# Optimization experiments

Measured on AMD Instinct MI355X. Metric: run time of the kernel, lower is better.

The kernel has to match this reference:

```python
import jax, jax.numpy as jnp
import numpy as np
from jax import lax


def _leaky(x):
    # LeakyReLU, negative_slope=0.1
    return jnp.where(x > 0, x, 0.1 * x)


def _conv(x, w, pad, groups=1):
    # NCHW / OIHW 2D conv, stride 1
    return lax.conv_general_dilated(
        x, w, (1, 1), [(pad, pad), (pad, pad)],
        dimension_numbers=("NCHW", "OIHW", "NCHW"),
        feature_group_count=groups)


def setup_inputs() -> dict:
    key = jax.random.key(0)
    ks = jax.random.split(key, 12)
    B, C, H, W = 16, 64, 256, 256
    KS = 3

    def nrm(k, shape, fan_in):
        return jax.random.normal(k, shape, jnp.float32) / np.float32(np.sqrt(fan_in))

    return {
        "x": jax.random.normal(ks[0], (B, C, H, W), jnp.float32),
        "t": jax.random.normal(ks[1], (B, 1, 1, 1), jnp.float32),
        # t_process: 1x1 convs (1->64, 64->64), no bias -> stored as matrices
        "tW1": nrm(ks[2], (C, 1), 1),
        "tW2": nrm(ks[3], (C, C), C),
        # f_process: two 3x3 convs 64->64 with bias
        "fW1": nrm(ks[4], (C, C, KS, KS), C * KS * KS),
        "fb1": jnp.zeros((C,), jnp.float32),
        "fW2": nrm(ks[5], (C, C, KS, KS), C * KS * KS),
        "fb2": jnp.zeros((C,), jnp.float32),
        # kernel branch: 1x1 convs (1->64, 64->64*9), no bias
        "kW1": nrm(ks[6], (C, 1), 1),
        "kW2": nrm(ks[7], (C * KS * KS, C), C),
        # conv33: 3x3 conv 64->64 with bias
        "cW": nrm(ks[8], (C, C, KS, KS), C * KS * KS),
        "cb": jnp.zeros((C,), jnp.float32),
    }


def reference(x, t, tW1, tW2, fW1, fb1, fW2, fb2, kW1, kW2, cW, cb):
    b, c, h, w = x.shape
    KS = 3

    # f_process: Conv3x3 -> LeakyReLU -> Conv3x3 -> LeakyReLU
    f = _leaky(_conv(x, fW1, 1) + fb1[None, :, None, None])
    f = _leaky(_conv(f, fW2, 1) + fb2[None, :, None, None])

    # t is (b,1,1,1); 1x1 convs on it are per-sample matmuls
    ts = t.reshape(b, 1)
    # t_process: Conv1x1 -> LeakyReLU -> Conv1x1 -> Sigmoid -> (b,c,1,1)
    mv = jax.nn.sigmoid(_leaky(ts @ tW1.T) @ tW2.T).reshape(b, c, 1, 1)

    # kernel branch: Conv1x1 -> LeakyReLU -> Conv1x1 -> LeakyReLU -> (b*c,1,3,3)
    kern = _leaky(_leaky(ts @ kW1.T) @ kW2.T).reshape(b * c, 1, KS, KS)

    # per-sample-channel dynamic depthwise conv: groups = b*c
    out = _conv(f.reshape(1, b * c, h, w), kern, (KS - 1) // 2,
                groups=b * c).reshape(b, c, h, w)

    # modulation gating + residual 3x3 conv
    return out * mv + _conv(x, cW, 1) + cb[None, :, None, None]
```

## Files before the change

kernel.cpp:

```cpp
#include <hip/hip_runtime.h>
#include <cstdint>

using short8  = __attribute__((ext_vector_type(8))) short;
using short4v = __attribute__((ext_vector_type(4))) short;
using f32x16  = __attribute__((ext_vector_type(16))) float;
using float4v = __attribute__((ext_vector_type(4))) float;
typedef unsigned short ushort_t;

#define CHUNK_ROW 520
#define CHUNK_SLOTS 1560
#define BUF_SLOTS 1632
#define BUF_SHORTS (BUF_SLOTS * 8)

__device__ __forceinline__ float lrelu(float x) { return x > 0.f ? x : 0.1f * x; }

__device__ __forceinline__ ushort_t f2bf(float f) {
    union { float f; unsigned u; } v; v.f = f;
    unsigned r = (v.u + 0x7FFFu + ((v.u >> 16) & 1u)) >> 16;
    return (ushort_t)r;
}
__device__ __forceinline__ float bf2f(ushort_t b) {
    union { unsigned u; float f; } v; v.u = ((unsigned)b) << 16; return v.f;
}

__device__ __forceinline__ void gload_lds16(const ushort_t* g, ushort_t* l) {
    __builtin_amdgcn_global_load_lds(
        (const __attribute__((address_space(1))) void*)g,
        (__attribute__((address_space(3))) void*)l, 16, 0, 0);
}

__global__ void k_tiny(const float* __restrict__ t, const float* __restrict__ tW1,
                       const float* __restrict__ tW2, const float* __restrict__ kW1,
                       const float* __restrict__ kW2, float* __restrict__ ktr) {
    int b = blockIdx.x;
    int c = threadIdx.x;
    __shared__ float h1[64], g1[64];
    float ts = t[b];
    h1[c] = lrelu(ts * tW1[c]);
    g1[c] = lrelu(ts * kW1[c]);
    __syncthreads();
    float s = 0.f;
    for (int j = 0; j < 64; ++j) s = fmaf(tW2[c * 64 + j], h1[j], s);
    float mvv = 1.f / (1.f + expf(-s));
    for (int q = 0; q < 9; ++q) {
        float s2 = 0.f;
        for (int j = 0; j < 64; ++j) s2 = fmaf(kW2[(c * 9 + q) * 64 + j], g1[j], s2);
        ktr[b * 576 + q * 64 + c] = lrelu(s2) * mvv;
    }
}

__global__ void k_zrow(ushort_t* __restrict__ z) {
    int i = blockIdx.x * 256 + threadIdx.x;
    *(short8*)(z + (size_t)i * 8) = (short8)0;
}

__global__ void k_pack(const float* __restrict__ w1, const float* __restrict__ w2,
                       const float* __restrict__ w3, ushort_t* __restrict__ wp) {
    int idx = blockIdx.x * 256 + threadIdx.x;
    if (idx >= 3 * 36864) return;
    int conv = idx / 36864, r = idx % 36864;
    const float* W = conv == 0 ? w1 : (conv == 1 ? w2 : w3);
    int j = r & 7, lane = (r >> 3) & 63, ct = (r >> 9) & 1, chunk = (r >> 10) & 3,
        t = r >> 12;
    int co = ct * 32 + (lane & 31);
    int ci = chunk * 16 + (lane >> 5) * 8 + j;
    wp[idx] = f2bf(W[(co * 64 + ci) * 9 + t]);
}

__global__ __launch_bounds__(256) void k_tr(const float* __restrict__ x,
                                            ushort_t* __restrict__ xbf) {
    int bid = blockIdx.x;
    int h = bid & 255, b = bid >> 8;
    int t = threadIdx.x;
    for (int it = 0; it < 8; ++it) {
        int idx = t + it * 256;
        int g = idx & 7, w = idx >> 3;
        const float* src = x + (((size_t)(b * 64 + g * 8) * 256 + h) * 256 + w);
        short8 v;
#pragma unroll
        for (int j = 0; j < 8; ++j) v[j] = (short)f2bf(src[(size_t)j * 65536]);
        *(short8*)(xbf + (((size_t)(b * 256 + h) * 256 + w) * 64 + g * 8)) = v;
    }
}

#define STAGE_CHUNK(chunk, bufbase)                                              \
    {                                                                            \
        _Pragma("unroll")                                                        \
        for (int i_ = 0; i_ < 7; ++i_) {                                         \
            int base_ = wv * 390 + i_ * 64;                                      \
            int S_ = base_ + lane;                                               \
            S_ = S_ < CHUNK_SLOTS ? S_ : CHUNK_SLOTS - 1;                        \
            int row_ = (S_ >= 2 * CHUNK_ROW) ? 2 : (S_ >= CHUNK_ROW ? 1 : 0);    \
            int rem_ = S_ - row_ * CHUNK_ROW;                                    \
            int mg_ = rem_ >> 3, sl_ = rem_ & 7;                                 \
            int sp_ = sl_ ^ (mg_ & 7);                                           \
            int p_ = mg_ * 4 + (sp_ >> 1), g_ = sp_ & 1;                         \
            int wsx_ = p_ - 1;                                                   \
            bool edge_ = (unsigned)wsx_ >= 256u;                                 \
            const ushort_t* rp_ = (row_ == 0) ? rb0 : (row_ == 1 ? rb1 : rb2);   \
            const ushort_t* src_ =                                               \
                edge_ ? zv : (rp_ + wsx_ * 64 + (chunk)*16 + g_ * 8);            \
            gload_lds16(src_, xs + (bufbase) + (size_t)base_ * 8);               \
        }                                                                        \
    }

#define VMCNT(n) asm volatile("s_waitcnt vmcnt(" #n ")" ::: "memory")
#define RBAR() __builtin_amdgcn_s_barrier()

__global__ __launch_bounds__(256, 2) void k_conv13(
    const ushort_t* __restrict__ in, const ushort_t* __restrict__ zv,
    const ushort_t* __restrict__ wpa, const ushort_t* __restrict__ wpc,
    const float* __restrict__ ba, const float* __restrict__ bc,
    ushort_t* __restrict__ f1out, float* __restrict__ cres) {
    __shared__ __align__(16) ushort_t xs[2 * BUF_SHORTS];
    const int tid = threadIdx.x;
    const int lane = tid & 63;
    const int wv = tid >> 6;
    const unsigned bid = blockIdx.x;
    const unsigned L = (bid & 7u) * 512u + (bid >> 3);
    const int h = L & 255, b = L >> 8;
    const int l31 = lane & 31, lhi = lane >> 5;
    const int pw0 = wv * 64;

    const ushort_t* rb0 = (h > 0)   ? in + ((size_t)(b * 256 + h - 1)) * 16384 : zv;
    const ushort_t* rb1 =             in + ((size_t)(b * 256 + h)) * 16384;
    const ushort_t* rb2 = (h < 255) ? in + ((size_t)(b * 256 + h + 1)) * 16384 : zv;

    f32x16 accA[2][2], accC[2][2];
#pragma unroll
    for (int a = 0; a < 2; ++a)
#pragma unroll
        for (int c = 0; c < 2; ++c) { accA[a][c] = (f32x16)0.0f; accC[a][c] = (f32x16)0.0f; }

#define COMPUTE13(chunk, bufbase)                                                   \
    {                                                                               \
        __builtin_amdgcn_s_setprio(1);                                              \
        _Pragma("unroll")                                                           \
        for (int t_ = 0; t_ < 9; ++t_) {                                            \
            const int dwx_ = t_ % 3, rr_ = t_ / 3;                                  \
            const int off_ = ((t_ * 4 + (chunk)) * 2) * 512 + lane * 8;             \
            short8 a0 = *(const short8*)(wpa + off_);                               \
            short8 a1 = *(const short8*)(wpa + off_ + 512);                         \
            short8 c0 = *(const short8*)(wpc + off_);                               \
            short8 c1 = *(const short8*)(wpc + off_ + 512);                         \
            _Pragma("unroll")                                                       \
            for (int pt_ = 0; pt_ < 2; ++pt_) {                                     \
                int p_ = pw0 + pt_ * 32 + l31 + dwx_;                               \
                int mg_ = p_ >> 2;                                                  \
                int sl_ = ((p_ & 3) * 2 + lhi) ^ (mg_ & 7);                         \
                short8 bf = *(const short8*)(                                       \
                    xs + (bufbase) + (size_t)(rr_ * CHUNK_ROW + mg_ * 8 + sl_) * 8);\
                accA[0][pt_] = __builtin_amdgcn_mfma_f32_32x32x16_bf16(a0, bf, accA[0][pt_], 0, 0, 0); \
                accA[1][pt_] = __builtin_amdgcn_mfma_f32_32x32x16_bf16(a1, bf, accA[1][pt_], 0, 0, 0); \
                accC[0][pt_] = __builtin_amdgcn_mfma_f32_32x32x16_bf16(c0, bf, accC[0][pt_], 0, 0, 0); \
                accC[1][pt_] = __builtin_amdgcn_mfma_f32_32x32x16_bf16(c1, bf, accC[1][pt_], 0, 0, 0); \
            }                                                                       \
        }                                                                           \
        __builtin_amdgcn_s_setprio(0);                                              \
    }

    STAGE_CHUNK(0, 0);
    STAGE_CHUNK(1, BUF_SHORTS);
    VMCNT(7);
    RBAR();
    COMPUTE13(0, 0);
    RBAR();
    STAGE_CHUNK(2, 0);
    VMCNT(7);
    RBAR();
    COMPUTE13(1, BUF_SHORTS);
    RBAR();
    STAGE_CHUNK(3, BUF_SHORTS);
    VMCNT(7);
    RBAR();
    COMPUTE13(2, 0);
    RBAR();
    VMCNT(0);
    RBAR();
    COMPUTE13(3, BUF_SHORTS);

    const int co_b = 4 * lhi;
    {
        ushort_t* outb = f1out + ((size_t)(b * 256 + h)) * 16384;
#pragma unroll
        for (int ct = 0; ct < 2; ++ct)
#pragma unroll
            for (int pt = 0; pt < 2; ++pt) {
                int pix = pw0 + pt * 32 + l31;
                ushort_t* po = outb + (size_t)pix * 64 + ct * 32 + co_b;
#pragma unroll
                for (int q = 0; q < 4; ++q) {
                    float4v bv = *(const float4v*)(ba + ct * 32 + co_b + 8 * q);
                    short4v sv;
#pragma unroll
                    for (int m = 0; m < 4; ++m) {
                        float v = lrelu(accA[ct][pt][q * 4 + m] + bv[m]);
                        sv[m] = (short)f2bf(v);
                    }
                    *(short4v*)(po + 8 * q) = sv;
                }
            }
    }
    {
        float* pb = cres + (((size_t)b * 64) << 16) + h * 256;
#pragma unroll
        for (int ct = 0; ct < 2; ++ct)
#pragma unroll
            for (int pt = 0; pt < 2; ++pt) {
                int pix = pw0 + pt * 32 + l31;
#pragma unroll
                for (int q = 0; q < 4; ++q) {
                    float4v bv = *(const float4v*)(bc + ct * 32 + co_b + 8 * q);
#pragma unroll
                    for (int m = 0; m < 4; ++m) {
                        int c = ct * 32 + co_b + 8 * q + m;
                        pb[((size_t)c << 16) + pix] = accC[ct][pt][q * 4 + m] + bv[m];
                    }
                }
            }
    }
#undef COMPUTE13
}

__global__ __launch_bounds__(256, 3) void k_conv2(const ushort_t* __restrict__ in,
                                                  const ushort_t* __restrict__ zv,
                                                  const ushort_t* __restrict__ wp,
                                                  const float* __restrict__ bias,
                                                  ushort_t* __restrict__ outp) {
    __shared__ __align__(16) ushort_t xs[2 * BUF_SHORTS];
    const int tid = threadIdx.x;
    const int lane = tid & 63;
    const int wv = tid >> 6;
    const unsigned bid = blockIdx.x;
    const unsigned L = (bid & 7u) * 512u + (bid >> 3);
    const int h = L & 255, b = L >> 8;
    const int l31 = lane & 31, lhi = lane >> 5;
    const int pw0 = wv * 64;

    const ushort_t* rb0 = (h > 0)   ? in + ((size_t)(b * 256 + h - 1)) * 16384 : zv;
    const ushort_t* rb1 =             in + ((size_t)(b * 256 + h)) * 16384;
    const ushort_t* rb2 = (h < 255) ? in + ((size_t)(b * 256 + h + 1)) * 16384 : zv;

    f32x16 acc[2][2];
#pragma unroll
    for (int a = 0; a < 2; ++a)
#pragma unroll
        for (int c = 0; c < 2; ++c) acc[a][c] = (f32x16)0.0f;

#define COMPUTE2(chunk, bufbase)                                                    \
    {                                                                               \
        __builtin_amdgcn_s_setprio(1);                                              \
        _Pragma("unroll")                                                           \
        for (int t_ = 0; t_ < 9; ++t_) {                                            \
            const int dwx_ = t_ % 3, rr_ = t_ / 3;                                  \
            const int off_ = ((t_ * 4 + (chunk)) * 2) * 512 + lane * 8;             \
            short8 a0 = *(const short8*)(wp + off_);                                \
            short8 a1 = *(const short8*)(wp + off_ + 512);                          \
            _Pragma("unroll")                                                       \
            for (int pt_ = 0; pt_ < 2; ++pt_) {                                     \
                int p_ = pw0 + pt_ * 32 + l31 + dwx_;                               \
                int mg_ = p_ >> 2;                                                  \
                int sl_ = ((p_ & 3) * 2 + lhi) ^ (mg_ & 7);                         \
                short8 bf = *(const short8*)(                                       \
                    xs + (bufbase) + (size_t)(rr_ * CHUNK_ROW + mg_ * 8 + sl_) * 8);\
                acc[0][pt_] = __builtin_amdgcn_mfma_f32_32x32x16_bf16(a0, bf, acc[0][pt_], 0, 0, 0); \
                acc[1][pt_] = __builtin_amdgcn_mfma_f32_32x32x16_bf16(a1, bf, acc[1][pt_], 0, 0, 0); \
            }                                                                       \
        }                                                                           \
        __builtin_amdgcn_s_setprio(0);                                              \
    }

    STAGE_CHUNK(0, 0);
    STAGE_CHUNK(1, BUF_SHORTS);
    VMCNT(7);
    RBAR();
    COMPUTE2(0, 0);
    RBAR();
    STAGE_CHUNK(2, 0);
    VMCNT(7);
    RBAR();
    COMPUTE2(1, BUF_SHORTS);
    RBAR();
    STAGE_CHUNK(3, BUF_SHORTS);
    VMCNT(7);
    RBAR();
    COMPUTE2(2, 0);
    RBAR();
    VMCNT(0);
    RBAR();
    COMPUTE2(3, BUF_SHORTS);

    const int co_b = 4 * lhi;
    ushort_t* pb = outp + (((size_t)b * 64) << 16) + h * 256;
#pragma unroll
    for (int ct = 0; ct < 2; ++ct)
#pragma unroll
        for (int pt = 0; pt < 2; ++pt) {
            int pix = pw0 + pt * 32 + l31;
#pragma unroll
            for (int q = 0; q < 4; ++q) {
                float4v bv = *(const float4v*)(bias + ct * 32 + co_b + 8 * q);
#pragma unroll
                for (int m = 0; m < 4; ++m) {
                    int c = ct * 32 + co_b + 8 * q + m;
                    float v = lrelu(acc[ct][pt][q * 4 + m] + bv[m]);
                    pb[((size_t)c << 16) + pix] = f2bf(v);
                }
            }
        }
#undef COMPUTE2
}

__global__ __launch_bounds__(256) void k_fin(const ushort_t* __restrict__ f2,
                                             const float* __restrict__ ktr,
                                             float* __restrict__ out) {
    __shared__ __align__(16) ushort_t s[10 * 272];
    const unsigned bid = blockIdx.x;
    const unsigned L = (bid & 7u) * 4096u + (bid >> 3);
    const int hb = L & 31, c = (L >> 5) & 63, b = L >> 11;
    const int h0 = hb * 8;
    const int w = threadIdx.x;

    const ushort_t* f2c = f2 + (((size_t)(b * 64 + c)) << 16);
    for (int i = w; i < 320; i += 256) {
        int r = i >> 5, seg = i & 31;
        int hs = h0 - 1 + r;
        short8 v = (short8)0;
        if ((unsigned)hs < 256u) v = *(const short8*)(f2c + hs * 256 + seg * 8);
        *(short8*)(&s[r * 272 + 8 + seg * 8]) = v;
        if (seg == 0) s[r * 272 + 7] = 0;
        if (seg == 31) s[r * 272 + 264] = 0;
    }
    __syncthreads();

    float kv[9];
#pragma unroll
    for (int t9 = 0; t9 < 9; ++t9) kv[t9] = ktr[b * 576 + t9 * 64 + c];

    float lv[10], cv[10], rv[10];
#pragma unroll
    for (int r = 0; r < 10; ++r) {
        lv[r] = bf2f(s[r * 272 + 7 + w]);
        cv[r] = bf2f(s[r * 272 + 8 + w]);
        rv[r] = bf2f(s[r * 272 + 9 + w]);
    }

    float* ob = out + (((size_t)(b * 64 + c)) << 16) + h0 * 256 + w;
#pragma unroll
    for (int rr = 0; rr < 8; ++rr) {
        float dwv = 0.f;
#pragma unroll
        for (int r3 = 0; r3 < 3; ++r3) {
            dwv = fmaf(kv[r3 * 3 + 0], lv[rr + r3], dwv);
            dwv = fmaf(kv[r3 * 3 + 1], cv[rr + r3], dwv);
            dwv = fmaf(kv[r3 * 3 + 2], rv[rr + r3], dwv);
        }
        float* po = ob + rr * 256;
        *po = *po + dwv;
    }
}

extern "C" void kernel_launch(void* const* d_in, const int* in_sizes, int n_in,
                              void* d_out, int out_size, void* d_ws, size_t ws_size,
                              hipStream_t stream) {
    const float* x   = (const float*)d_in[0];
    const float* t   = (const float*)d_in[1];
    const float* tW1 = (const float*)d_in[2];
    const float* tW2 = (const float*)d_in[3];
    const float* fW1 = (const float*)d_in[4];
    const float* fb1 = (const float*)d_in[5];
    const float* fW2 = (const float*)d_in[6];
    const float* fb2 = (const float*)d_in[7];
    const float* kW1 = (const float*)d_in[8];
    const float* kW2 = (const float*)d_in[9];
    const float* cW  = (const float*)d_in[10];
    const float* cb  = (const float*)d_in[11];

    char* ws = (char*)d_ws;
    float*    ktr  = (float*)ws;
    ushort_t* wp   = (ushort_t*)(ws + 65536);
    ushort_t* zv   = (ushort_t*)(ws + 294912);
    ushort_t* xbf  = (ushort_t*)(ws + (512u << 10));
    ushort_t* f1bf = (ushort_t*)(ws + (512u << 10) + ((size_t)128 << 20));
    ushort_t* f2n  = xbf;
    float*    out  = (float*)d_out;

    k_tiny<<<dim3(16), dim3(64), 0, stream>>>(t, tW1, tW2, kW1, kW2, ktr);
    k_zrow<<<dim3(8), dim3(256), 0, stream>>>(zv);
    k_pack<<<dim3((3 * 36864 + 255) / 256), dim3(256), 0, stream>>>(fW1, fW2, cW, wp);
    k_tr<<<dim3(4096), dim3(256), 0, stream>>>(x, xbf);

    k_conv13<<<dim3(4096), dim3(256), 0, stream>>>(
        xbf, zv, wp, wp + 2 * 36864, fb1, cb, f1bf, out);
    k_conv2<<<dim3(4096), dim3(256), 0, stream>>>(f1bf, zv, wp + 36864, fb2, f2n);
    k_fin<<<dim3(32768), dim3(256), 0, stream>>>(f2n, ktr, out);
}
```

Baseline: 631.1 us.

## Compute two output rows per block and stage conv weights in LDS

Both 3x3 conv kernels now use 512-thread blocks that compute two adjacent output rows. They stage four input rows, so the shared rows are reused, and the block count is halved. Conv weights are repacked into chunk-major layout and loaded into LDS via global_load_lds (double-buffered per chunk for the fused conv1/conv3 kernel, fully resident for conv2) instead of being read from global memory by every wave. The aim is to cut redundant input-row and weight reads. The cost is much larger dynamic LDS, which may limit occupancy, and added barrier coordination.

```diff
diff --git a/kernel.cpp b/kernel.cpp
--- a/kernel.cpp
+++ b/kernel.cpp
@@ -7,10 +7,14 @@
 using float4v = __attribute__((ext_vector_type(4))) float;
 typedef unsigned short ushort_t;
 
-#define CHUNK_ROW 520
-#define CHUNK_SLOTS 1560
-#define BUF_SLOTS 1632
-#define BUF_SHORTS (BUF_SLOTS * 8)
+#define CSLOTS 2080
+#define BSLOTS 2144
+#define XSH (BSLOTS * 8)
+#define WROWS 40
+#define WCH (WROWS * 512)
+#define W1SH 36864
+#define DYN13 ((2 * WCH + 2 * XSH) * 2)
+#define DYN2  ((W1SH + 2 * XSH) * 2)
 
 __device__ __forceinline__ float lrelu(float x) { return x > 0.f ? x : 0.1f * x; }
 
@@ -28,6 +32,10 @@
         (const __attribute__((address_space(1))) void*)g,
         (__attribute__((address_space(3))) void*)l, 16, 0, 0);
 }
+
+#define VMCNT(n) asm volatile("s_waitcnt vmcnt(" #n ")" ::: "memory")
+#define RBAR() __builtin_amdgcn_s_barrier()
+#define SCHED0() __builtin_amdgcn_sched_barrier(0)
 
 __global__ void k_tiny(const float* __restrict__ t, const float* __restrict__ tW1,
                        const float* __restrict__ tW2, const float* __restrict__ kW1,
@@ -55,16 +63,37 @@
 }
 
 __global__ void k_pack(const float* __restrict__ w1, const float* __restrict__ w2,
-                       const float* __restrict__ w3, ushort_t* __restrict__ wp) {
+                       const float* __restrict__ w3, ushort_t* __restrict__ wpM,
+                       ushort_t* __restrict__ wp2) {
     int idx = blockIdx.x * 256 + threadIdx.x;
-    if (idx >= 3 * 36864) return;
-    int conv = idx / 36864, r = idx % 36864;
-    const float* W = conv == 0 ? w1 : (conv == 1 ? w2 : w3);
-    int j = r & 7, lane = (r >> 3) & 63, ct = (r >> 9) & 1, chunk = (r >> 10) & 3,
-        t = r >> 12;
+    const int NM = 4 * 36 * 512;
+    if (idx >= NM + 4 * 18 * 512) return;
+    const float* W;
+    ushort_t* dst;
+    int chunk, row;
+    int e;
+    if (idx < NM) {
+        chunk = idx / (36 * 512);
+        int rem = idx % (36 * 512);
+        row = rem / 512;
+        e = rem % 512;
+        W = (row < 18) ? w1 : w3;
+        dst = wpM + idx;
+        row %= 18;
+    } else {
+        int i2 = idx - NM;
+        chunk = i2 / (18 * 512);
+        int rem = i2 % (18 * 512);
+        row = rem / 512;
+        e = rem % 512;
+        W = w2;
+        dst = wp2 + i2;
+    }
+    int lane = e >> 3, j = e & 7;
+    int t = row >> 1, ct = row & 1;
     int co = ct * 32 + (lane & 31);
     int ci = chunk * 16 + (lane >> 5) * 8 + j;
-    wp[idx] = f2bf(W[(co * 64 + ci) * 9 + t]);
+    *dst = f2bf(W[(co * 64 + ci) * 9 + t]);
 }
 
 __global__ __launch_bounds__(256) void k_tr(const float* __restrict__ x,
@@ -83,48 +112,93 @@
     }
 }
 
-#define STAGE_CHUNK(chunk, bufbase)                                              \
+#define STAGE_X(chunk, xbase)                                                    \
     {                                                                            \
         _Pragma("unroll")                                                        \
-        for (int i_ = 0; i_ < 7; ++i_) {                                         \
-            int base_ = wv * 390 + i_ * 64;                                      \
+        for (int i_ = 0; i_ < 5; ++i_) {                                         \
+            int base_ = wv * 260 + i_ * 64;                                      \
             int S_ = base_ + lane;                                               \
-            S_ = S_ < CHUNK_SLOTS ? S_ : CHUNK_SLOTS - 1;                        \
-            int row_ = (S_ >= 2 * CHUNK_ROW) ? 2 : (S_ >= CHUNK_ROW ? 1 : 0);    \
-            int rem_ = S_ - row_ * CHUNK_ROW;                                    \
+            S_ = S_ < CSLOTS ? S_ : CSLOTS - 1;                                  \
+            int r_ = (S_ >= 1560) ? 3 : ((S_ >= 1040) ? 2 : ((S_ >= 520) ? 1 : 0)); \
+            int rem_ = S_ - r_ * 520;                                            \
             int mg_ = rem_ >> 3, sl_ = rem_ & 7;                                 \
             int sp_ = sl_ ^ (mg_ & 7);                                           \
             int p_ = mg_ * 4 + (sp_ >> 1), g_ = sp_ & 1;                         \
             int wsx_ = p_ - 1;                                                   \
             bool edge_ = (unsigned)wsx_ >= 256u;                                 \
-            const ushort_t* rp_ = (row_ == 0) ? rb0 : (row_ == 1 ? rb1 : rb2);   \
+            const ushort_t* rp_ =                                                \
+                (r_ == 0) ? rb0 : ((r_ == 1) ? rb1 : ((r_ == 2) ? rb2 : rb3));   \
             const ushort_t* src_ =                                               \
                 edge_ ? zv : (rp_ + wsx_ * 64 + (chunk)*16 + g_ * 8);            \
-            gload_lds16(src_, xs + (bufbase) + (size_t)base_ * 8);               \
+            gload_lds16(src_, xs + (xbase) + (size_t)base_ * 8);                 \
         }                                                                        \
     }
 
-#define VMCNT(n) asm volatile("s_waitcnt vmcnt(" #n ")" ::: "memory")
-#define RBAR() __builtin_amdgcn_s_barrier()
-
-__global__ __launch_bounds__(256, 2) void k_conv13(
+#define STAGE_W(chunk, wbase)                                                    \
+    {                                                                            \
+        _Pragma("unroll")                                                        \
+        for (int i_ = 0; i_ < 5; ++i_) {                                         \
+            int row_ = wv * 5 + i_;                                              \
+            int rc_ = row_ > 35 ? 35 : row_;                                     \
+            gload_lds16(wpM + (size_t)((chunk)*36 + rc_) * 512 + lane * 8,       \
+                        wlds + (wbase) + (size_t)row_ * 512);                    \
+        }                                                                        \
+    }
+
+__device__ __forceinline__ void computeM(const ushort_t* __restrict__ wlds,
+                                         const ushort_t* __restrict__ xs,
+                                         int wbase, int xbase, int lane, int pw0,
+                                         int l31, int lhi, int rbase,
+                                         f32x16 (&accA)[2][2], f32x16 (&accC)[2][2]) {
+    __builtin_amdgcn_s_setprio(1);
+#pragma unroll
+    for (int t = 0; t < 9; ++t) {
+        short8 a0 = *(const short8*)(wlds + wbase + (size_t)(t * 2 + 0) * 512 + lane * 8);
+        short8 a1 = *(const short8*)(wlds + wbase + (size_t)(t * 2 + 1) * 512 + lane * 8);
+        short8 c0 = *(const short8*)(wlds + wbase + (size_t)(18 + t * 2 + 0) * 512 + lane * 8);
+        short8 c1 = *(const short8*)(wlds + wbase + (size_t)(18 + t * 2 + 1) * 512 + lane * 8);
+        const int dwx = t % 3, rr = t / 3;
+        const int rowIdx = rbase + rr;
+#pragma unroll
+        for (int pt = 0; pt < 2; ++pt) {
+            int p = pw0 + pt * 32 + l31 + dwx;
+            int mg = p >> 2;
+            int sl = ((p & 3) * 2 + lhi) ^ (mg & 7);
+            short8 bf = *(const short8*)(
+                xs + xbase + (size_t)(rowIdx * 520 + mg * 8 + sl) * 8);
+            accA[0][pt] = __builtin_amdgcn_mfma_f32_32x32x16_bf16(a0, bf, accA[0][pt], 0, 0, 0);
+            accA[1][pt] = __builtin_amdgcn_mfma_f32_32x32x16_bf16(a1, bf, accA[1][pt], 0, 0, 0);
+            accC[0][pt] = __builtin_amdgcn_mfma_f32_32x32x16_bf16(c0, bf, accC[0][pt], 0, 0, 0);
+            accC[1][pt] = __builtin_amdgcn_mfma_f32_32x32x16_bf16(c1, bf, accC[1][pt], 0, 0, 0);
+        }
+    }
+    __builtin_amdgcn_s_setprio(0);
+}
+
+__global__ __launch_bounds__(512, 2) void k_conv13M(
     const ushort_t* __restrict__ in, const ushort_t* __restrict__ zv,
-    const ushort_t* __restrict__ wpa, const ushort_t* __restrict__ wpc,
-    const float* __restrict__ ba, const float* __restrict__ bc,
-    ushort_t* __restrict__ f1out, float* __restrict__ cres) {
-    __shared__ __align__(16) ushort_t xs[2 * BUF_SHORTS];
+    const ushort_t* __restrict__ wpM, const float* __restrict__ ba,
+    const float* __restrict__ bc, ushort_t* __restrict__ f1out,
+    float* __restrict__ cres) {
+    extern __shared__ char smem_raw[];
+    ushort_t* wlds = (ushort_t*)smem_raw;
+    ushort_t* xs = wlds + 2 * WCH;
+
     const int tid = threadIdx.x;
     const int lane = tid & 63;
     const int wv = tid >> 6;
     const unsigned bid = blockIdx.x;
-    const unsigned L = (bid & 7u) * 512u + (bid >> 3);
-    const int h = L & 255, b = L >> 8;
+    const unsigned L = (bid & 7u) * 256u + (bid >> 3);
+    const int h0 = (L & 127) * 2, b = L >> 7;
     const int l31 = lane & 31, lhi = lane >> 5;
-    const int pw0 = wv * 64;
-
-    const ushort_t* rb0 = (h > 0)   ? in + ((size_t)(b * 256 + h - 1)) * 16384 : zv;
-    const ushort_t* rb1 =             in + ((size_t)(b * 256 + h)) * 16384;
-    const ushort_t* rb2 = (h < 255) ? in + ((size_t)(b * 256 + h + 1)) * 16384 : zv;
+    const int pw0 = (wv & 3) * 64;
+    const int rbase = wv >> 2;
+    const int ro = h0 + rbase;
+
+    const ushort_t* rb0 = (h0 > 0)   ? in + ((size_t)(b * 256 + h0 - 1)) * 16384 : zv;
+    const ushort_t* rb1 =              in + ((size_t)(b * 256 + h0)) * 16384;
+    const ushort_t* rb2 =              in + ((size_t)(b * 256 + h0 + 1)) * 16384;
+    const ushort_t* rb3 = (h0 < 254) ? in + ((size_t)(b * 256 + h0 + 2)) * 16384 : zv;
 
     f32x16 accA[2][2], accC[2][2];
 #pragma unroll
@@ -132,56 +206,28 @@
 #pragma unroll
         for (int c = 0; c < 2; ++c) { accA[a][c] = (f32x16)0.0f; accC[a][c] = (f32x16)0.0f; }
 
-#define COMPUTE13(chunk, bufbase)                                                   \
-    {                                                                               \
-        __builtin_amdgcn_s_setprio(1);                                              \
-        _Pragma("unroll")                                                           \
-        for (int t_ = 0; t_ < 9; ++t_) {                                            \
-            const int dwx_ = t_ % 3, rr_ = t_ / 3;                                  \
-            const int off_ = ((t_ * 4 + (chunk)) * 2) * 512 + lane * 8;             \
-            short8 a0 = *(const short8*)(wpa + off_);                               \
-            short8 a1 = *(const short8*)(wpa + off_ + 512);                         \
-            short8 c0 = *(const short8*)(wpc + off_);                               \
-            short8 c1 = *(const short8*)(wpc + off_ + 512);                         \
-            _Pragma("unroll")                                                       \
-            for (int pt_ = 0; pt_ < 2; ++pt_) {                                     \
-                int p_ = pw0 + pt_ * 32 + l31 + dwx_;                               \
-                int mg_ = p_ >> 2;                                                  \
-                int sl_ = ((p_ & 3) * 2 + lhi) ^ (mg_ & 7);                         \
-                short8 bf = *(const short8*)(                                       \
-                    xs + (bufbase) + (size_t)(rr_ * CHUNK_ROW + mg_ * 8 + sl_) * 8);\
-                accA[0][pt_] = __builtin_amdgcn_mfma_f32_32x32x16_bf16(a0, bf, accA[0][pt_], 0, 0, 0); \
-                accA[1][pt_] = __builtin_amdgcn_mfma_f32_32x32x16_bf16(a1, bf, accA[1][pt_], 0, 0, 0); \
-                accC[0][pt_] = __builtin_amdgcn_mfma_f32_32x32x16_bf16(c0, bf, accC[0][pt_], 0, 0, 0); \
-                accC[1][pt_] = __builtin_amdgcn_mfma_f32_32x32x16_bf16(c1, bf, accC[1][pt_], 0, 0, 0); \
-            }                                                                       \
-        }                                                                           \
-        __builtin_amdgcn_s_setprio(0);                                              \
-    }
-
-    STAGE_CHUNK(0, 0);
-    STAGE_CHUNK(1, BUF_SHORTS);
-    VMCNT(7);
+    STAGE_W(0, 0); STAGE_X(0, 0);
+    STAGE_W(1, WCH); STAGE_X(1, XSH);
+    VMCNT(10);
+    RBAR(); SCHED0();
+    computeM(wlds, xs, 0, 0, lane, pw0, l31, lhi, rbase, accA, accC);
     RBAR();
-    COMPUTE13(0, 0);
+    STAGE_W(2, 0); STAGE_X(2, 0);
+    VMCNT(10);
+    RBAR(); SCHED0();
+    computeM(wlds, xs, WCH, XSH, lane, pw0, l31, lhi, rbase, accA, accC);
     RBAR();
-    STAGE_CHUNK(2, 0);
-    VMCNT(7);
-    RBAR();
-    COMPUTE13(1, BUF_SHORTS);
-    RBAR();
-    STAGE_CHUNK(3, BUF_SHORTS);
-    VMCNT(7);
-    RBAR();
-    COMPUTE13(2, 0);
-    RBAR();
+    STAGE_W(3, WCH); STAGE_X(3, XSH);
+    VMCNT(10);
+    RBAR(); SCHED0();
+    computeM(wlds, xs, 0, 0, lane, pw0, l31, lhi, rbase, accA, accC);
     VMCNT(0);
-    RBAR();
-    COMPUTE13(3, BUF_SHORTS);
+    RBAR(); SCHED0();
+    computeM(wlds, xs, WCH, XSH, lane, pw0, l31, lhi, rbase, accA, accC);
 
     const int co_b = 4 * lhi;
     {
-        ushort_t* outb = f1out + ((size_t)(b * 256 + h)) * 16384;
+        ushort_t* outb = f1out + ((size_t)(b * 256 + ro)) * 16384;
 #pragma unroll
         for (int ct = 0; ct < 2; ++ct)
 #pragma unroll
@@ -202,7 +248,7 @@
             }
     }
     {
-        float* pb = cres + (((size_t)b * 64) << 16) + h * 256;
+        float* pb = cres + (((size_t)b * 64) << 16) + ro * 256;
 #pragma unroll
         for (int ct = 0; ct < 2; ++ct)
 #pragma unroll
@@ -219,27 +265,31 @@
                 }
             }
     }
-#undef COMPUTE13
-}
-
-__global__ __launch_bounds__(256, 3) void k_conv2(const ushort_t* __restrict__ in,
-                                                  const ushort_t* __restrict__ zv,
-                                                  const ushort_t* __restrict__ wp,
-                                                  const float* __restrict__ bias,
-                                                  ushort_t* __restrict__ outp) {
-    __shared__ __align__(16) ushort_t xs[2 * BUF_SHORTS];
+}
+
+__global__ __launch_bounds__(512, 2) void k_conv2(
+    const ushort_t* __restrict__ in, const ushort_t* __restrict__ zv,
+    const ushort_t* __restrict__ wp2, const float* __restrict__ bias,
+    ushort_t* __restrict__ outp) {
+    extern __shared__ char smem_raw[];
+    ushort_t* wlds = (ushort_t*)smem_raw;
+    ushort_t* xs = wlds + W1SH;
+
     const int tid = threadIdx.x;
     const int lane = tid & 63;
     const int wv = tid >> 6;
     const unsigned bid = blockIdx.x;
-    const unsigned L = (bid & 7u) * 512u + (bid >> 3);
-    const int h = L & 255, b = L >> 8;
+    const unsigned L = (bid & 7u) * 256u + (bid >> 3);
+    const int h0 = (L & 127) * 2, b = L >> 7;
     const int l31 = lane & 31, lhi = lane >> 5;
-    const int pw0 = wv * 64;
-
-    const ushort_t* rb0 = (h > 0)   ? in + ((size_t)(b * 256 + h - 1)) * 16384 : zv;
-    const ushort_t* rb1 =             in + ((size_t)(b * 256 + h)) * 16384;
-    const ushort_t* rb2 = (h < 255) ? in + ((size_t)(b * 256 + h + 1)) * 16384 : zv;
+    const int pw0 = (wv & 3) * 64;
+    const int rbase = wv >> 2;
+    const int ro = h0 + rbase;
+
+    const ushort_t* rb0 = (h0 > 0)   ? in + ((size_t)(b * 256 + h0 - 1)) * 16384 : zv;
+    const ushort_t* rb1 =              in + ((size_t)(b * 256 + h0)) * 16384;
+    const ushort_t* rb2 =              in + ((size_t)(b * 256 + h0 + 1)) * 16384;
+    const ushort_t* rb3 = (h0 < 254) ? in + ((size_t)(b * 256 + h0 + 2)) * 16384 : zv;
 
     f32x16 acc[2][2];
 #pragma unroll
@@ -247,22 +297,22 @@
 #pragma unroll
         for (int c = 0; c < 2; ++c) acc[a][c] = (f32x16)0.0f;
 
-#define COMPUTE2(chunk, bufbase)                                                    \
+#define COMPUTE2(chunk, xbase)                                                      \
     {                                                                               \
         __builtin_amdgcn_s_setprio(1);                                              \
         _Pragma("unroll")                                                           \
         for (int t_ = 0; t_ < 9; ++t_) {                                            \
+            short8 a0 = *(const short8*)(wlds + (size_t)((chunk)*18 + t_ * 2) * 512 + lane * 8); \
+            short8 a1 = *(const short8*)(wlds + (size_t)((chunk)*18 + t_ * 2 + 1) * 512 + lane * 8); \
             const int dwx_ = t_ % 3, rr_ = t_ / 3;                                  \
-            const int off_ = ((t_ * 4 + (chunk)) * 2) * 512 + lane * 8;             \
-            short8 a0 = *(const short8*)(wp + off_);                                \
-            short8 a1 = *(const short8*)(wp + off_ + 512);                          \
+            const int rowIdx_ = rbase + rr_;                                        \
             _Pragma("unroll")                                                       \
             for (int pt_ = 0; pt_ < 2; ++pt_) {                                     \
                 int p_ = pw0 + pt_ * 32 + l31 + dwx_;                               \
                 int mg_ = p_ >> 2;                                                  \
                 int sl_ = ((p_ & 3) * 2 + lhi) ^ (mg_ & 7);                         \
                 short8 bf = *(const short8*)(                                       \
-                    xs + (bufbase) + (size_t)(rr_ * CHUNK_ROW + mg_ * 8 + sl_) * 8);\
+                    xs + (xbase) + (size_t)(rowIdx_ * 520 + mg_ * 8 + sl_) * 8);    \
                 acc[0][pt_] = __builtin_amdgcn_mfma_f32_32x32x16_bf16(a0, bf, acc[0][pt_], 0, 0, 0); \
                 acc[1][pt_] = __builtin_amdgcn_mfma_f32_32x32x16_bf16(a1, bf, acc[1][pt_], 0, 0, 0); \
             }                                                                       \
@@ -270,28 +320,33 @@
         __builtin_amdgcn_s_setprio(0);                                              \
     }
 
-    STAGE_CHUNK(0, 0);
-    STAGE_CHUNK(1, BUF_SHORTS);
-    VMCNT(7);
-    RBAR();
+#pragma unroll
+    for (int i = 0; i < 9; ++i) {
+        int idx = wv * 9 + i;
+        gload_lds16(wp2 + (size_t)idx * 512 + lane * 8, wlds + (size_t)idx * 512);
+    }
+    STAGE_X(0, 0);
+    STAGE_X(1, XSH);
+    VMCNT(5);
+    RBAR(); SCHED0();
     COMPUTE2(0, 0);
     RBAR();
-    STAGE_CHUNK(2, 0);
-    VMCNT(7);
+    STAGE_X(2, 0);
+    VMCNT(5);
+    RBAR(); SCHED0();
+    COMPUTE2(1, XSH);
     RBAR();
-    COMPUTE2(1, BUF_SHORTS);
-    RBAR();
-    STAGE_CHUNK(3, BUF_SHORTS);
-    VMCNT(7);
-    RBAR();
+    STAGE_X(3, XSH);
+    VMCNT(5);
+    RBAR(); SCHED0();
     COMPUTE2(2, 0);
-    RBAR();
     VMCNT(0);
-    RBAR();
-    COMPUTE2(3, BUF_SHORTS);
+    RBAR(); SCHED0();
+    COMPUTE2(3, XSH);
+#undef COMPUTE2
 
     const int co_b = 4 * lhi;
-    ushort_t* pb = outp + (((size_t)b * 64) << 16) + h * 256;
+    ushort_t* pb = outp + (((size_t)b * 64) << 16) + ro * 256;
 #pragma unroll
     for (int ct = 0; ct < 2; ++ct)
 #pragma unroll
@@ -308,7 +363,6 @@
                 }
             }
         }
-#undef COMPUTE2
 }
 
 __global__ __launch_bounds__(256) void k_fin(const ushort_t* __restrict__ f2,
@@ -378,20 +432,27 @@
 
     char* ws = (char*)d_ws;
     float*    ktr  = (float*)ws;
-    ushort_t* wp   = (ushort_t*)(ws + 65536);
+    ushort_t* wpM  = (ushort_t*)(ws + 65536);
+    ushort_t* wp2  = wpM + 4 * 36 * 512;
     ushort_t* zv   = (ushort_t*)(ws + 294912);
     ushort_t* xbf  = (ushort_t*)(ws + (512u << 10));
     ushort_t* f1bf = (ushort_t*)(ws + (512u << 10) + ((size_t)128 << 20));
     ushort_t* f2n  = xbf;
     float*    out  = (float*)d_out;
 
+    hipFuncSetAttribute(reinterpret_cast<const void*>(&k_conv13M),
+                        hipFuncAttributeMaxDynamicSharedMemorySize, DYN13);
+    hipFuncSetAttribute(reinterpret_cast<const void*>(&k_conv2),
+                        hipFuncAttributeMaxDynamicSharedMemorySize, DYN2);
+
     k_tiny<<<dim3(16), dim3(64), 0, stream>>>(t, tW1, tW2, kW1, kW2, ktr);
     k_zrow<<<dim3(8), dim3(256), 0, stream>>>(zv);
-    k_pack<<<dim3((3 * 36864 + 255) / 256), dim3(256), 0, stream>>>(fW1, fW2, cW, wp);
+    k_pack<<<dim3((4 * 36 * 512 + 4 * 18 * 512 + 255) / 256), dim3(256), 0, stream>>>(
+        fW1, fW2, cW, wpM, wp2);
     k_tr<<<dim3(4096), dim3(256), 0, stream>>>(x, xbf);
 
-    k_conv13<<<dim3(4096), dim3(256), 0, stream>>>(
-        xbf, zv, wp, wp + 2 * 36864, fb1, cb, f1bf, out);
-    k_conv2<<<dim3(4096), dim3(256), 0, stream>>>(f1bf, zv, wp + 36864, fb2, f2n);
+    k_conv13M<<<dim3(2048), dim3(512), DYN13, stream>>>(
+        xbf, zv, wpM, fb1, cb, f1bf, out);
+    k_conv2<<<dim3(2048), dim3(512), DYN2, stream>>>(f1bf, zv, wp2, fb2, f2n);
     k_fin<<<dim3(32768), dim3(256), 0, stream>>>(f2n, ktr, out);
 }
```

Result: no change. 635.1 us (+0.6%).
